# Optimization experiments

Measured on AMD Instinct MI355X. Metric: run time of the kernel, lower is better.

## Reference

```python
import jax, jax.numpy as jnp
import numpy as np
from jax import lax

CHANNEL = 64
HIDDEN = 128

def _conv(x, w, b):
    # x: [B, Cin, H, W], w: [Cout, Cin, 3, 3] -> [B, Cout, H, W], SAME padding
    y = lax.conv_general_dilated(x, w, window_strides=(1, 1), padding='SAME',
                                 dimension_numbers=('NCHW', 'OIHW', 'NCHW'))
    return y + b[None, :, None, None]

def setup_inputs() -> dict:
    key = jax.random.key(0)
    ks = jax.random.split(key, 5)
    T, B, C, H, W = 12, 2, CHANNEL, 128, 128
    x = jax.random.normal(ks[0], (T, B, C, H, W), dtype=jnp.float32)
    fan_g = (C + HIDDEN) * 9
    W_gates = jax.random.normal(ks[1], (4 * HIDDEN, C + HIDDEN, 3, 3), dtype=jnp.float32) / np.sqrt(fan_g)
    b_gates = jnp.zeros((4 * HIDDEN,), dtype=jnp.float32)
    W_out = jax.random.normal(ks[2], (C, HIDDEN, 3, 3), dtype=jnp.float32) / np.sqrt(HIDDEN * 9)
    b_out = jnp.zeros((C,), dtype=jnp.float32)
    return {'x': x, 'W_gates': W_gates, 'b_gates': b_gates, 'W_out': W_out, 'b_out': b_out}

def _convlstm_forward(x, W_gates, b_gates, W_out, b_out):
    T, B, C, H, W = x.shape
    h0 = jnp.zeros((B, HIDDEN, H, W), dtype=x.dtype)
    c0 = jnp.zeros((B, HIDDEN, H, W), dtype=x.dtype)

    def step(carry, xt):
        h, c = carry
        gates = _conv(jnp.concatenate([xt, h], axis=1), W_gates, b_gates)
        i_g, f_g, o_g, g_g = jnp.split(gates, 4, axis=1)
        c = jax.nn.sigmoid(f_g) * c + jax.nn.sigmoid(i_g) * jnp.tanh(g_g)
        h = jax.nn.sigmoid(o_g) * jnp.tanh(c)
        return (h, c), h

    _, hs = lax.scan(step, (h0, c0), x)          # hs: [T, B, HIDDEN, H, W]
    out = _conv(hs.reshape(T * B, HIDDEN, H, W), W_out, b_out)
    return out.reshape(T, B, C, H, W)

def reference(x, W_gates, b_gates, W_out, b_out):
    return _convlstm_forward(x, W_gates, b_gates, W_out, b_out)
```

## Files before the change

### kernel.cpp

```cpp
#include <hip/hip_runtime.h>

typedef _Float16 f16;
typedef __attribute__((ext_vector_type(8))) _Float16 f16x8;
typedef __attribute__((ext_vector_type(4))) _Float16 f16x4;
typedef __attribute__((ext_vector_type(4))) float f32x4;

#define SLICE_H 4326400


__device__ __forceinline__ void gld_lds16(void* lds, const void* g) {
  __builtin_amdgcn_global_load_lds(
      (const __attribute__((address_space(1))) void*)g,
      (__attribute__((address_space(3))) void*)lds, 16, 0, 0);
}

__device__ __forceinline__ float sigf(float v) { return 1.0f / (1.0f + __expf(-v)); }
__device__ __forceinline__ float tanh_fast(float v) { return 2.0f / (1.0f + __expf(-2.0f * v)) - 1.0f; }


__global__ __launch_bounds__(256) void kwt(const float* __restrict__ wsrc,
                                           f16* __restrict__ th, int R) {
  int idx = blockIdx.x * 256 + threadIdx.x;
  if (idx >= 9 * R) return;
  int tap = idx / R, r = idx - tap * R;
  th[idx] = (f16)wsrc[(size_t)r * 9 + tap];
}

__global__ __launch_bounds__(256) void kwtg(const float* __restrict__ wsrc,
                                            f16* __restrict__ th) {
  int idx = blockIdx.x * 256 + threadIdx.x;
  const int R = 512 * 192;
  if (idx >= 9 * R) return;
  int tap = idx / R, rr = idx - tap * R;
  int co = rr / 192, ci = rr - co * 192;
  int gate = co >> 7, hch = co & 127;
  int N = ((hch >> 6) << 8) + (((hch & 63) >> 4) << 6) + (gate << 4) + (hch & 15);
  th[(size_t)tap * R + (size_t)N * 192 + ci] = (f16)wsrc[(size_t)rr * 9 + tap];
}


__global__ __launch_bounds__(256) void kxform(const float* __restrict__ xt,
                                              f16* __restrict__ xp) {
  int pid = blockIdx.x * 256 + threadIdx.x;
  int b = pid >> 14, y = (pid >> 7) & 127, x = pid & 127;
  const float* src = xt + (size_t)b * 64 * 16384 + (size_t)y * 128 + x;
  size_t doff = ((size_t)((b * 130 + y + 1) * 130 + (x + 1))) * 64;
#pragma unroll
  for (int cc = 0; cc < 8; ++cc) {
    f16x8 vh;
#pragma unroll
    for (int j = 0; j < 8; ++j) vh[j] = (f16)src[(size_t)(cc * 8 + j) * 16384];
    *(f16x8*)(xp + doff + cc * 8) = vh;
  }
}


#define SMEM_G (25344 + 49152)

__global__ __launch_bounds__(256, 2) void kgates(
    const f16* __restrict__ xp, const f16* __restrict__ hp,
    const f16* __restrict__ wg, const float* __restrict__ bg,
    float* __restrict__ cbuf, f16* __restrict__ hslot) {
  extern __shared__ char smem[];
  f16* Ap = (f16*)smem;
  f16* Br = (f16*)(smem + 25344);
  const int tid = threadIdx.x;
  const int lane = tid & 63;
  const int w = tid >> 6;
  const int y = blockIdx.x;
  const int b = blockIdx.y;
  const int z = blockIdx.z;
  const int n0 = z * 256;
  const int chunk = (lane & 3) ^ ((lane >> 3) & 3);

  f32x4 acc[8][4] = {};

  auto stageA = [&](int cig) {
    const f16* S; int CS, cigl;
    if (cig < 2) { S = xp; CS = 64;  cigl = cig; }
    else         { S = hp; CS = 128; cigl = cig - 2; }
    for (int i = w; i < 27; i += 4) {
      int dy = i / 9, sub = i - dy * 9;
      int xp0 = sub * 16;
      const f16* src = S +
          ((size_t)((b * 130 + y + dy) * 130 + xp0 + (lane >> 2))) * CS +
          cigl * 32 + chunk * 8;
      f16* dst = Ap + (dy * 132 + xp0) * 32;
      if (sub == 8) { if (lane < 16) gld_lds16(dst, src); }
      else gld_lds16(dst, src);
    }
  };
  auto stageB = [&](int cig, int tap, int slot) {
    f16* dst = Br + slot * 8192;
    for (int i = w; i < 16; i += 4) {
      const f16* src = wg +
          ((size_t)(tap * 512 + n0 + i * 16 + (lane >> 2))) * 192 +
          cig * 32 + chunk * 8;
      gld_lds16(dst + i * 512, src);
    }
  };

  stageA(0);
  stageB(0, 0, 0);
  stageB(0, 1, 1);
  asm volatile("s_waitcnt vmcnt(4)" ::: "memory");
  __builtin_amdgcn_s_barrier();

  int sl = 0;
  for (int cig = 0; cig < 6; ++cig) {
    for (int tap = 0; tap < 9; ++tap) {
      const int j = cig * 9 + tap;
      const int dy = tap / 3, dx = tap - dy * 3;
      const int q = lane >> 4;
      const f16* Bc = Br + sl * 8192;
      f16x8 af[8], bfr[4];
#pragma unroll
      for (int mf = 0; mf < 8; ++mf) {
        int r = mf * 16 + (lane & 15) + dx;
        af[mf] = *(const f16x8*)(Ap + (dy * 132 + r) * 32 + ((q ^ ((r >> 1) & 3)) << 3));
      }
#pragma unroll
      for (int nf = 0; nf < 4; ++nf) {
        int n = w * 64 + nf * 16 + (lane & 15);
        bfr[nf] = *(const f16x8*)(Bc + n * 32 + ((q ^ ((n >> 1) & 3)) << 3));
      }
      if (j + 2 < 54) {
        int j2 = j + 2;
        stageB(j2 / 9, j2 % 9, (sl + 2 >= 3) ? sl - 1 : sl + 2);
      }
      __builtin_amdgcn_s_setprio(1);
#pragma unroll
      for (int mf = 0; mf < 8; ++mf)
#pragma unroll
        for (int nf = 0; nf < 4; ++nf)
          acc[mf][nf] = __builtin_amdgcn_mfma_f32_16x16x32_f16(af[mf], bfr[nf], acc[mf][nf], 0, 0, 0);
      __builtin_amdgcn_s_setprio(0);
      if (tap == 8) {
        __builtin_amdgcn_s_barrier();
        if (cig < 5) stageA(cig + 1);
        asm volatile("s_waitcnt vmcnt(0)" ::: "memory");
        __builtin_amdgcn_s_barrier();
      } else {
        if (j + 2 < 54) asm volatile("s_waitcnt vmcnt(4)" ::: "memory");
        else            asm volatile("s_waitcnt vmcnt(0)" ::: "memory");
        __builtin_amdgcn_s_barrier();
      }
      sl = (sl + 1 >= 3) ? 0 : sl + 1;
    }
  }

  const int lch = w * 16 + (lane & 15);
  const int hch = z * 64 + lch;
  const float bi  = bg[hch];
  const float bf2 = bg[128 + hch];
  const float bo2 = bg[256 + hch];
  const float bg2 = bg[384 + hch];
  const size_t pixbase = ((size_t)(b * 128 + y)) * 128;
  const size_t hbase = ((size_t)((b * 130 + y + 1) * 130 + 1)) * 128 + hch;
#pragma unroll
  for (int mf = 0; mf < 8; ++mf) {
#pragma unroll
    for (int r = 0; r < 4; ++r) {
      int px = mf * 16 + (lane >> 4) * 4 + r;
      size_t cidx = (pixbase + px) * 128 + hch;
      float co = cbuf[cidx];
      float iv = sigf(acc[mf][0][r] + bi);
      float fv = sigf(acc[mf][1][r] + bf2);
      float ov = sigf(acc[mf][2][r] + bo2);
      float gv = tanh_fast(acc[mf][3][r] + bg2);
      float cv = fv * co + iv * gv;
      cbuf[cidx] = cv;
      hslot[hbase + (size_t)px * 128] = (f16)(ov * tanh_fast(cv));
    }
  }
}


#define SMEM_O (25344 + 12288)

__global__ __launch_bounds__(256, 4) void koutconv(
    const f16* __restrict__ hr, int slot0, const f16* __restrict__ wo,
    const float* __restrict__ bo, float* __restrict__ outb) {
  extern __shared__ char smem[];
  f16* Ap = (f16*)smem;
  f16* Br = (f16*)(smem + 25344);
  const int tid = threadIdx.x, lane = tid & 63, w = tid >> 6;
  const int y = blockIdx.x;
  const int b = blockIdx.y;
  const int ts = blockIdx.z;
  const f16* hp = hr + (size_t)((slot0 + ts) % 5) * SLICE_H;
  float* outt = outb + (size_t)ts * 2 * 64 * 16384;
  const int chunk = (lane & 3) ^ ((lane >> 3) & 3);

  f32x4 acc[2][4] = {};

  auto stageA = [&](int cig) {
    for (int i = w; i < 27; i += 4) {
      int dy = i / 9, sub = i - dy * 9;
      int xp0 = sub * 16;
      const f16* src = hp +
          ((size_t)((b * 130 + y + dy) * 130 + xp0 + (lane >> 2))) * 128 +
          cig * 32 + chunk * 8;
      f16* dst = Ap + (dy * 132 + xp0) * 32;
      if (sub == 8) { if (lane < 16) gld_lds16(dst, src); }
      else gld_lds16(dst, src);
    }
  };
  auto stageB = [&](int j, int slot) {
    int cig = j / 9, tap = j - cig * 9;
    const f16* src = wo +
        ((size_t)(tap * 64 + w * 16 + (lane >> 2))) * 128 +
        cig * 32 + chunk * 8;
    gld_lds16(Br + slot * 2048 + w * 512, src);
  };

  stageA(0);
  stageB(0, 0);
  stageB(1, 1);
  asm volatile("s_waitcnt vmcnt(1)" ::: "memory");
  __builtin_amdgcn_s_barrier();

  int sl = 0;
  for (int cig = 0; cig < 4; ++cig) {
    for (int tap = 0; tap < 9; ++tap) {
      const int j = cig * 9 + tap;
      const int dy = tap / 3, dx = tap - dy * 3;
      const int q = lane >> 4;
      const f16* Bc = Br + sl * 2048;
      f16x8 af[2], bfr[4];
#pragma unroll
      for (int mf = 0; mf < 2; ++mf) {
        int r = w * 32 + mf * 16 + (lane & 15) + dx;
        af[mf] = *(const f16x8*)(Ap + (dy * 132 + r) * 32 + ((q ^ ((r >> 1) & 3)) << 3));
      }
#pragma unroll
      for (int nf = 0; nf < 4; ++nf) {
        int n = nf * 16 + (lane & 15);
        bfr[nf] = *(const f16x8*)(Bc + n * 32 + ((q ^ ((n >> 1) & 3)) << 3));
      }
      if (j + 2 < 36) stageB(j + 2, (sl + 2 >= 3) ? sl - 1 : sl + 2);
      __builtin_amdgcn_s_setprio(1);
#pragma unroll
      for (int mf = 0; mf < 2; ++mf)
#pragma unroll
        for (int nf = 0; nf < 4; ++nf)
          acc[mf][nf] = __builtin_amdgcn_mfma_f32_16x16x32_f16(af[mf], bfr[nf], acc[mf][nf], 0, 0, 0);
      __builtin_amdgcn_s_setprio(0);
      if (tap == 8) {
        __builtin_amdgcn_s_barrier();
        if (cig < 3) stageA(cig + 1);
        asm volatile("s_waitcnt vmcnt(0)" ::: "memory");
        __builtin_amdgcn_s_barrier();
      } else {
        if (j + 2 < 36) asm volatile("s_waitcnt vmcnt(1)" ::: "memory");
        else            asm volatile("s_waitcnt vmcnt(0)" ::: "memory");
        __builtin_amdgcn_s_barrier();
      }
      sl = (sl + 1 >= 3) ? 0 : sl + 1;
    }
  }

#pragma unroll
  for (int nf = 0; nf < 4; ++nf) {
    int cout = nf * 16 + (lane & 15);
    float bias = bo[cout];
#pragma unroll
    for (int mf = 0; mf < 2; ++mf) {
      int xbase = w * 32 + mf * 16 + (lane >> 4) * 4;
      f32x4 v = acc[mf][nf];
      v[0] += bias; v[1] += bias; v[2] += bias; v[3] += bias;
      *(f32x4*)(outt + (((size_t)b * 64 + cout) * 128 + y) * 128 + xbase) = v;
    }
  }
}


extern "C" void kernel_launch(void* const* d_in, const int* in_sizes, int n_in,
                              void* d_out, int out_size, void* d_ws, size_t ws_size,
                              hipStream_t stream) {
  const float* x  = (const float*)d_in[0];
  const float* Wg = (const float*)d_in[1];
  const float* bg = (const float*)d_in[2];
  const float* Wo = (const float*)d_in[3];
  const float* bo = (const float*)d_in[4];
  float* out = (float*)d_out;

  char* base = (char*)d_ws;
  size_t off = 0;
  auto carve = [&](size_t bytes) {
    char* p = base + off;
    off += (bytes + 1023) & ~(size_t)1023;
    return p;
  };
  const size_t PADPOS = (size_t)2 * 130 * 130;
  const size_t xpad_b  = PADPOS * 64 * 2 + 1024;
  const size_t hring_b = (size_t)5 * SLICE_H * 2 + 1024;
  const size_t c_b = (size_t)2 * 128 * 128 * 128 * 4;

  f16* xp    = (f16*)carve(xpad_b);
  f16* hr    = (f16*)carve(hring_b);
  float* cbuf = (float*)carve(c_b);
  f16* wg    = (f16*)carve((size_t)9 * 512 * 192 * 2);
  f16* wo    = (f16*)carve((size_t)9 * 64 * 128 * 2);

  hipMemsetAsync(xp, 0, xpad_b, stream);
  hipMemsetAsync(hr, 0, hring_b, stream);
  hipMemsetAsync(cbuf, 0, c_b, stream);

  kwtg<<<(9 * 512 * 192 + 255) / 256, 256, 0, stream>>>(Wg, wg);
  kwt<<<(9 * 64 * 128 + 255) / 256, 256, 0, stream>>>(Wo, wo, 64 * 128);

  for (int t = 0; t < 12; ++t) {
    const float* xt = x + (size_t)t * 2 * 64 * 16384;
    kxform<<<128, 256, 0, stream>>>(xt, xp);
    kgates<<<dim3(128, 2, 2), 256, SMEM_G, stream>>>(
        xp, hr + (size_t)(t % 5) * SLICE_H, wg, bg, cbuf,
        hr + (size_t)((t + 1) % 5) * SLICE_H);
    if ((t & 3) == 3) {
      koutconv<<<dim3(128, 2, 4), 256, SMEM_O, stream>>>(
          hr, (t - 2) % 5, wo, bo, out + (size_t)(t - 3) * 2 * 64 * 16384);
    }
  }
}
```

Measured before the change: 1.032 ms.

## Compute two output rows per gates block with 8 waves sharing weight tiles

The gates kernel now processes two image rows per block using 512 threads (8 waves arranged 2x4), so each staged weight tile in LDS is reused across both rows and weight traffic per output halves. The A staging loads four input rows instead of three, and the MFMA loop is split into two half-passes separated by extra barriers, apparently to interleave LDS reads with MFMA work. The grid is halved to match. In exchange it adds more barriers per iteration, uses more LDS per block, and the launch bound of 2 blocks of 512 threads raises register pressure.

```diff
diff --git a/kernel.cpp b/kernel.cpp
--- a/kernel.cpp
+++ b/kernel.cpp
@@ -55,22 +55,23 @@
 }
 
 
-#define SMEM_G (25344 + 49152)
-
-__global__ __launch_bounds__(256, 2) void kgates(
+#define SMEM_G (33792 + 49152)
+
+__global__ __launch_bounds__(512, 2) void kgates(
     const f16* __restrict__ xp, const f16* __restrict__ hp,
     const f16* __restrict__ wg, const float* __restrict__ bg,
     float* __restrict__ cbuf, f16* __restrict__ hslot) {
   extern __shared__ char smem[];
   f16* Ap = (f16*)smem;
-  f16* Br = (f16*)(smem + 25344);
+  f16* Br = (f16*)(smem + 33792);
   const int tid = threadIdx.x;
   const int lane = tid & 63;
   const int w = tid >> 6;
-  const int y = blockIdx.x;
+  const int y0 = blockIdx.x * 2;
   const int b = blockIdx.y;
   const int z = blockIdx.z;
   const int n0 = z * 256;
+  const int wm = w >> 2, wn = w & 3;
   const int chunk = (lane & 3) ^ ((lane >> 3) & 3);
 
   f32x4 acc[8][4] = {};
@@ -79,20 +80,21 @@
     const f16* S; int CS, cigl;
     if (cig < 2) { S = xp; CS = 64;  cigl = cig; }
     else         { S = hp; CS = 128; cigl = cig - 2; }
-    for (int i = w; i < 27; i += 4) {
-      int dy = i / 9, sub = i - dy * 9;
+    for (int i = w; i < 36; i += 8) {
+      int dyg = i / 9, sub = i - dyg * 9;
       int xp0 = sub * 16;
       const f16* src = S +
-          ((size_t)((b * 130 + y + dy) * 130 + xp0 + (lane >> 2))) * CS +
+          ((size_t)((b * 130 + y0 + dyg) * 130 + xp0 + (lane >> 2))) * CS +
           cigl * 32 + chunk * 8;
-      f16* dst = Ap + (dy * 132 + xp0) * 32;
+      f16* dst = Ap + (dyg * 132 + xp0) * 32;
       if (sub == 8) { if (lane < 16) gld_lds16(dst, src); }
       else gld_lds16(dst, src);
     }
   };
-  auto stageB = [&](int cig, int tap, int slot) {
-    f16* dst = Br + slot * 8192;
-    for (int i = w; i < 16; i += 4) {
+  auto stageB = [&](int j) {
+    int cig = j / 9, tap = j - cig * 9;
+    f16* dst = Br + (j % 3) * 8192;
+    for (int i = w; i < 16; i += 8) {
       const f16* src = wg +
           ((size_t)(tap * 512 + n0 + i * 16 + (lane >> 2))) * 192 +
           cig * 32 + chunk * 8;
@@ -101,62 +103,74 @@
   };
 
   stageA(0);
-  stageB(0, 0, 0);
-  stageB(0, 1, 1);
-  asm volatile("s_waitcnt vmcnt(4)" ::: "memory");
+  stageB(0);
+  stageB(1);
+  asm volatile("s_waitcnt vmcnt(2)" ::: "memory");
   __builtin_amdgcn_s_barrier();
 
-  int sl = 0;
-  for (int cig = 0; cig < 6; ++cig) {
-    for (int tap = 0; tap < 9; ++tap) {
-      const int j = cig * 9 + tap;
-      const int dy = tap / 3, dx = tap - dy * 3;
-      const int q = lane >> 4;
-      const f16* Bc = Br + sl * 8192;
-      f16x8 af[8], bfr[4];
-#pragma unroll
-      for (int mf = 0; mf < 8; ++mf) {
-        int r = mf * 16 + (lane & 15) + dx;
-        af[mf] = *(const f16x8*)(Ap + (dy * 132 + r) * 32 + ((q ^ ((r >> 1) & 3)) << 3));
-      }
-#pragma unroll
-      for (int nf = 0; nf < 4; ++nf) {
-        int n = w * 64 + nf * 16 + (lane & 15);
-        bfr[nf] = *(const f16x8*)(Bc + n * 32 + ((q ^ ((n >> 1) & 3)) << 3));
-      }
-      if (j + 2 < 54) {
-        int j2 = j + 2;
-        stageB(j2 / 9, j2 % 9, (sl + 2 >= 3) ? sl - 1 : sl + 2);
-      }
-      __builtin_amdgcn_s_setprio(1);
-#pragma unroll
-      for (int mf = 0; mf < 8; ++mf)
-#pragma unroll
-        for (int nf = 0; nf < 4; ++nf)
-          acc[mf][nf] = __builtin_amdgcn_mfma_f32_16x16x32_f16(af[mf], bfr[nf], acc[mf][nf], 0, 0, 0);
-      __builtin_amdgcn_s_setprio(0);
-      if (tap == 8) {
-        __builtin_amdgcn_s_barrier();
-        if (cig < 5) stageA(cig + 1);
-        asm volatile("s_waitcnt vmcnt(0)" ::: "memory");
-        __builtin_amdgcn_s_barrier();
-      } else {
-        if (j + 2 < 54) asm volatile("s_waitcnt vmcnt(4)" ::: "memory");
-        else            asm volatile("s_waitcnt vmcnt(0)" ::: "memory");
-        __builtin_amdgcn_s_barrier();
-      }
-      sl = (sl + 1 >= 3) ? 0 : sl + 1;
-    }
-  }
-
-  const int lch = w * 16 + (lane & 15);
-  const int hch = z * 64 + lch;
+  for (int j = 0; j < 54; ++j) {
+    const int cig = j / 9, tap = j - cig * 9;
+    const int dy = tap / 3, dx = tap - dy * 3;
+    const int q = lane >> 4;
+    const f16* Bc = Br + (j % 3) * 8192;
+    const f16* Arow = Ap + (wm + dy) * (132 * 32);
+    f16x8 af0[4], af1[4], bfr[4];
+
+#pragma unroll
+    for (int mf = 0; mf < 4; ++mf) {
+      int r = mf * 16 + (lane & 15) + dx;
+      af0[mf] = *(const f16x8*)(Arow + r * 32 + ((q ^ ((r >> 1) & 3)) << 3));
+    }
+#pragma unroll
+    for (int nf = 0; nf < 4; ++nf) {
+      int n = wn * 64 + nf * 16 + (lane & 15);
+      bfr[nf] = *(const f16x8*)(Bc + n * 32 + ((q ^ ((n >> 1) & 3)) << 3));
+    }
+    if (j + 2 < 54) stageB(j + 2);
+    __builtin_amdgcn_s_barrier();
+    __builtin_amdgcn_s_setprio(1);
+#pragma unroll
+    for (int mf = 0; mf < 4; ++mf)
+#pragma unroll
+      for (int nf = 0; nf < 4; ++nf)
+        acc[mf][nf] = __builtin_amdgcn_mfma_f32_16x16x32_f16(af0[mf], bfr[nf], acc[mf][nf], 0, 0, 0);
+    __builtin_amdgcn_s_setprio(0);
+    __builtin_amdgcn_s_barrier();
+
+#pragma unroll
+    for (int mf = 0; mf < 4; ++mf) {
+      int r = (mf + 4) * 16 + (lane & 15) + dx;
+      af1[mf] = *(const f16x8*)(Arow + r * 32 + ((q ^ ((r >> 1) & 3)) << 3));
+    }
+    __builtin_amdgcn_s_barrier();
+    __builtin_amdgcn_s_setprio(1);
+#pragma unroll
+    for (int mf = 0; mf < 4; ++mf)
+#pragma unroll
+      for (int nf = 0; nf < 4; ++nf)
+        acc[mf + 4][nf] = __builtin_amdgcn_mfma_f32_16x16x32_f16(af1[mf], bfr[nf], acc[mf + 4][nf], 0, 0, 0);
+    __builtin_amdgcn_s_setprio(0);
+
+    if (tap == 8) {
+      __builtin_amdgcn_s_barrier();
+      if (cig < 5) stageA(cig + 1);
+      asm volatile("s_waitcnt vmcnt(0)" ::: "memory");
+      __builtin_amdgcn_s_barrier();
+    } else {
+      if (j + 2 < 54) asm volatile("s_waitcnt vmcnt(2)" ::: "memory");
+      else            asm volatile("s_waitcnt vmcnt(0)" ::: "memory");
+      __builtin_amdgcn_s_barrier();
+    }
+  }
+
+  const int hch = z * 64 + wn * 16 + (lane & 15);
   const float bi  = bg[hch];
   const float bf2 = bg[128 + hch];
   const float bo2 = bg[256 + hch];
   const float bg2 = bg[384 + hch];
-  const size_t pixbase = ((size_t)(b * 128 + y)) * 128;
-  const size_t hbase = ((size_t)((b * 130 + y + 1) * 130 + 1)) * 128 + hch;
+  const int yr = y0 + wm;
+  const size_t pixbase = ((size_t)(b * 128 + yr)) * 128;
+  const size_t hbase = ((size_t)((b * 130 + yr + 1) * 130 + 1)) * 128 + hch;
 #pragma unroll
   for (int mf = 0; mf < 8; ++mf) {
 #pragma unroll
@@ -313,7 +327,7 @@
   for (int t = 0; t < 12; ++t) {
     const float* xt = x + (size_t)t * 2 * 64 * 16384;
     kxform<<<128, 256, 0, stream>>>(xt, xp);
-    kgates<<<dim3(128, 2, 2), 256, SMEM_G, stream>>>(
+    kgates<<<dim3(64, 2, 2), 512, SMEM_G, stream>>>(
         xp, hr + (size_t)(t % 5) * SLICE_H, wg, bg, cbuf,
         hr + (size_t)((t + 1) % 5) * SLICE_H);
     if ((t & 3) == 3) {
```

Result: slower. 1.084 ms (+5.0%).
